# Kernel tuning notes

Measured on AMD Instinct MI355X. Metric: run time of the kernel, lower is better.

## Reference

```python
import jax, jax.numpy as jnp
import numpy as np

VOCAB, EMB_DIM, HIDDEN, NUM_CLASSES = 50000, 300, 1000, 5
B, MAX_LEN = 4096, 128


def setup_inputs() -> dict:
    key = jax.random.key(0)
    k1, k2, k3, k4, k5, k6, k7 = jax.random.split(key, 7)
    x = jax.random.randint(k1, (B, MAX_LEN), 0, VOCAB, dtype=jnp.int64)
    lengths = jnp.maximum(jax.random.randint(k2, (B,), 0, MAX_LEN, dtype=jnp.int64), 1)
    emb_table = jax.random.normal(k3, (VOCAB, EMB_DIM), dtype=jnp.float32) * 0.1
    W1 = jax.random.normal(k4, (2 * EMB_DIM, HIDDEN), dtype=jnp.float32) * (1.0 / np.sqrt(2 * EMB_DIM))
    b1 = jax.random.normal(k5, (HIDDEN,), dtype=jnp.float32) * 0.01
    W2 = jax.random.normal(k6, (HIDDEN, NUM_CLASSES), dtype=jnp.float32) * (1.0 / np.sqrt(HIDDEN))
    b2 = jax.random.normal(k7, (NUM_CLASSES,), dtype=jnp.float32) * 0.01
    return {"x": x, "lengths": lengths, "emb_table": emb_table,
            "W1": W1, "b1": b1, "W2": W2, "b2": b2}


def reference(x, lengths, emb_table, W1, b1, W2, b2):
    emb = emb_table[x]                                  # [B, L, D] gather
    mask = (jnp.arange(emb.shape[1])[None, :] < lengths[:, None])  # [B, L]
    m = mask[:, :, None].astype(emb.dtype)
    avg_pool = jnp.sum(emb * m, axis=1) / lengths[:, None].astype(emb.dtype)  # [B, D]
    neg_inf = jnp.finfo(emb.dtype).min
    max_pool = jnp.max(jnp.where(mask[:, :, None], emb, neg_inf), axis=1)     # [B, D]
    rep = jnp.concatenate([avg_pool, max_pool], axis=1)  # [B, 2D]
    hidden = jax.nn.relu(rep @ W1 + b1)                  # [B, 1000]
    logits = hidden @ W2 + b2                            # [B, C]
    return logits
```

## Files before the change

### kernel.cpp

```cpp
#include <hip/hip_runtime.h>
#include <float.h>
#include <stdint.h>

#define EMB_DIM  300
#define MAX_LEN  128
#define HIDDEN   1000
#define NCLS     5
#define VOCAB_SZ 50000
#define KPAD     640
#define NPAD     1024

typedef float    f32x4  __attribute__((ext_vector_type(4)));
typedef __bf16   bf16x8 __attribute__((ext_vector_type(8)));
typedef unsigned short ushort8v __attribute__((ext_vector_type(8)));

__device__ __forceinline__ unsigned short f2bf(float f) {
    union { float f; uint32_t u; } v; v.f = f;
    uint32_t u = v.u;
    return (unsigned short)((u + 0x7FFFu + ((u >> 16) & 1u)) >> 16);
}
__device__ __forceinline__ float bf2f(unsigned short h) {
    union { uint32_t u; float f; } v; v.u = ((uint32_t)h) << 16;
    return v.f;
}

__global__ __launch_bounds__(256) void transpose_w1(
    const float* __restrict__ W1, unsigned short* __restrict__ Bt)
{
    __shared__ float t[32][33];
    const int tx = threadIdx.x & 31, ty = threadIdx.x >> 5;
    const int n0 = blockIdx.x * 32, k0 = blockIdx.y * 32;
    #pragma unroll
    for (int i = 0; i < 4; ++i) {
        int k = k0 + ty + i * 8, n = n0 + tx;
        t[ty + i * 8][tx] = (k < 600 && n < HIDDEN) ? W1[(size_t)k * HIDDEN + n] : 0.f;
    }
    __syncthreads();
    #pragma unroll
    for (int i = 0; i < 4; ++i) {
        int n = n0 + ty + i * 8, k = k0 + tx;
        Bt[(size_t)n * KPAD + k] = f2bf(t[tx][ty + i * 8]);
    }
}

__global__ __launch_bounds__(128) void pool_kernel(
    const int* __restrict__ x, const int* __restrict__ lengths,
    const float* __restrict__ emb, unsigned short* __restrict__ rep)
{
    const int b = blockIdx.x;
    const int t = threadIdx.x;

    __shared__ int sidx[MAX_LEN];
    sidx[t] = x[b * MAX_LEN + t];
    __syncthreads();

    unsigned short* rb = rep + (size_t)b * KPAD;

    if (t >= 75) {
        if (t < 85) {
            ushort4 z = {0, 0, 0, 0};
            *(ushort4*)(rb + 600 + (t - 75) * 4) = z;
        }
        return;
    }

    int L = lengths[b];
    L = max(1, min(L, MAX_LEN));

    const int d = t * 4;
    float4 s  = {0.f, 0.f, 0.f, 0.f};
    float4 mx = {-FLT_MAX, -FLT_MAX, -FLT_MAX, -FLT_MAX};

    for (int i = 0; i < L; ++i) {
        int idx = sidx[i];
        idx = max(0, min(idx, VOCAB_SZ - 1));
        const float4 v = *(const float4*)(emb + (size_t)idx * EMB_DIM + d);
        s.x += v.x; s.y += v.y; s.z += v.z; s.w += v.w;
        mx.x = fmaxf(mx.x, v.x); mx.y = fmaxf(mx.y, v.y);
        mx.z = fmaxf(mx.z, v.z); mx.w = fmaxf(mx.w, v.w);
    }

    const float inv = 1.0f / (float)L;
    ushort4 av, mv;
    av.x = f2bf(s.x * inv); av.y = f2bf(s.y * inv);
    av.z = f2bf(s.z * inv); av.w = f2bf(s.w * inv);
    mv.x = f2bf(mx.x); mv.y = f2bf(mx.y); mv.z = f2bf(mx.z); mv.w = f2bf(mx.w);
    *(ushort4*)(rb + d)       = av;
    *(ushort4*)(rb + 300 + d) = mv;
}

#define BM 64
#define BN 64
#define BK 32

__global__ __launch_bounds__(256, 4) void gemm1_mfma(
    const unsigned short* __restrict__ A,
    const unsigned short* __restrict__ Bt,
    const float* __restrict__ bias,
    unsigned short* __restrict__ H,
    int M)
{
    __shared__ unsigned short As[2][BM * BK];
    __shared__ unsigned short Bs[2][BN * BK];

    const int tid  = threadIdx.x;
    const int wv   = tid >> 6;
    const int lane = tid & 63;
    const int bm   = blockIdx.y * BM;
    const int bn   = blockIdx.x * BN;
    const int wr   = (wv & 1) * 32;
    const int wc   = (wv >> 1) * 32;

    f32x4 acc[2][2] = {};

    auto stage = [&](int buf, int k0) {
        {
            int ci  = wv * 64 + lane;
            int row = ci >> 2, c = ci & 3;
            const unsigned short* g = A + (size_t)(bm + row) * KPAD + k0 + c * 8;
            unsigned short* l = &As[buf][wv * 512];
            __builtin_amdgcn_global_load_lds(g, l, 16, 0, 0);
        }
        {
            int ci  = wv * 64 + lane;
            int row = ci >> 2, c = ci & 3;
            const unsigned short* g = Bt + (size_t)(bn + row) * KPAD + k0 + c * 8;
            unsigned short* l = &Bs[buf][wv * 512];
            __builtin_amdgcn_global_load_lds(g, l, 16, 0, 0);
        }
    };

    stage(0, 0);
    int cur = 0;
    const int q = lane >> 4, r16 = lane & 15;

    #pragma unroll 1
    for (int it = 0; it < KPAD / BK; ++it) {
        __syncthreads();
        if (it + 1 < KPAD / BK) stage(cur ^ 1, (it + 1) * BK);

        bf16x8 af[2], bfr[2];
        #pragma unroll
        for (int mi = 0; mi < 2; ++mi)
            af[mi] = *(const bf16x8*)&As[cur][(wr + mi * 16 + r16) * BK + q * 8];
        #pragma unroll
        for (int nj = 0; nj < 2; ++nj)
            bfr[nj] = *(const bf16x8*)&Bs[cur][(wc + nj * 16 + r16) * BK + q * 8];
        #pragma unroll
        for (int mi = 0; mi < 2; ++mi)
            #pragma unroll
            for (int nj = 0; nj < 2; ++nj)
                acc[mi][nj] = __builtin_amdgcn_mfma_f32_16x16x32_bf16(
                    af[mi], bfr[nj], acc[mi][nj], 0, 0, 0);
        cur ^= 1;
    }

    #pragma unroll
    for (int nj = 0; nj < 2; ++nj) {
        int n = bn + wc + nj * 16 + r16;
        if (n >= HIDDEN) continue;
        float bv = bias[n];
        #pragma unroll
        for (int mi = 0; mi < 2; ++mi) {
            #pragma unroll
            for (int r = 0; r < 4; ++r) {
                int m = bm + wr + mi * 16 + q * 4 + r;
                float v = acc[mi][nj][r] + bv;
                H[(size_t)m * HIDDEN + n] = f2bf(fmaxf(v, 0.f));
            }
        }
    }
}

__global__ __launch_bounds__(256) void gemm2_kernel(
    const unsigned short* __restrict__ Hb,
    const float* __restrict__ W2,
    const float* __restrict__ b2,
    float* __restrict__ out)
{
    const int wv   = threadIdx.x >> 6;
    const int lane = threadIdx.x & 63;
    const int b    = blockIdx.x * 4 + wv;
    const unsigned short* hr = Hb + (size_t)b * HIDDEN;

    float acc[NCLS] = {0.f, 0.f, 0.f, 0.f, 0.f};
    #pragma unroll
    for (int c = 0; c < 2; ++c) {
        int k0 = c * 512 + lane * 8;
        if (k0 + 8 <= HIDDEN) {
            ushort8v hv = *(const ushort8v*)(hr + k0);
            #pragma unroll
            for (int j = 0; j < 8; ++j) {
                float h = bf2f(hv[j]);
                const float* w = W2 + (size_t)(k0 + j) * NCLS;
                #pragma unroll
                for (int cc = 0; cc < NCLS; ++cc) acc[cc] += h * w[cc];
            }
        }
    }
    #pragma unroll
    for (int off = 32; off > 0; off >>= 1)
        #pragma unroll
        for (int cc = 0; cc < NCLS; ++cc)
            acc[cc] += __shfl_down(acc[cc], off, 64);

    if (lane == 0) {
        #pragma unroll
        for (int cc = 0; cc < NCLS; ++cc)
            out[(size_t)b * NCLS + cc] = acc[cc] + b2[cc];
    }
}

extern "C" void kernel_launch(void* const* d_in, const int* in_sizes, int n_in,
                              void* d_out, int out_size, void* d_ws, size_t ws_size,
                              hipStream_t stream)
{
    const int*   x       = (const int*)d_in[0];
    const int*   lengths = (const int*)d_in[1];
    const float* emb     = (const float*)d_in[2];
    const float* W1      = (const float*)d_in[3];
    const float* b1      = (const float*)d_in[4];
    const float* W2      = (const float*)d_in[5];
    const float* b2      = (const float*)d_in[6];
    float*       out     = (float*)d_out;

    const int B = in_sizes[1];

    unsigned short* rep    = (unsigned short*)d_ws;
    unsigned short* w1t    = rep + (size_t)B * KPAD;
    unsigned short* hidden = w1t + (size_t)NPAD * KPAD;

    transpose_w1<<<dim3(32, 20), 256, 0, stream>>>(W1, w1t);
    pool_kernel<<<B, 128, 0, stream>>>(x, lengths, emb, rep);

    dim3 g1(NPAD / BN, B / BM);
    gemm1_mfma<<<g1, 256, 0, stream>>>(rep, w1t, b1, hidden, B);

    gemm2_kernel<<<B / 4, 256, 0, stream>>>(hidden, W2, b2, out);
}
```

Before: 167.1 us.

## Gather pooling from a bf16 copy of the embedding table and bf16 W2

```diff
diff --git a/kernel.cpp b/kernel.cpp
--- a/kernel.cpp
+++ b/kernel.cpp
@@ -9,6 +9,7 @@
 #define VOCAB_SZ 50000
 #define KPAD     640
 #define NPAD     1024
+#define EMBPAD   320
 
 typedef float    f32x4  __attribute__((ext_vector_type(4)));
 typedef __bf16   bf16x8 __attribute__((ext_vector_type(8)));
@@ -24,6 +25,22 @@
     return v.f;
 }
 
+__global__ __launch_bounds__(256) void convert_emb(
+    const float* __restrict__ emb, unsigned short* __restrict__ embb)
+{
+    const int i = blockIdx.x * 256 + threadIdx.x;
+    const int total = VOCAB_SZ * (EMBPAD / 4);
+    if (i >= total) return;
+    const int v  = i / (EMBPAD / 4);
+    const int ch = i - v * (EMBPAD / 4);
+    ushort4 o = {0, 0, 0, 0};
+    if (ch < 75) {
+        const float4 f = *(const float4*)(emb + (size_t)v * EMB_DIM + ch * 4);
+        o.x = f2bf(f.x); o.y = f2bf(f.y); o.z = f2bf(f.z); o.w = f2bf(f.w);
+    }
+    *(ushort4*)(embb + (size_t)v * EMBPAD + ch * 4) = o;
+}
+
 __global__ __launch_bounds__(256) void transpose_w1(
     const float* __restrict__ W1, unsigned short* __restrict__ Bt)
 {
@@ -43,9 +60,19 @@
     }
 }
 
-__global__ __launch_bounds__(128) void pool_kernel(
+__global__ __launch_bounds__(256) void transpose_w2(
+    const float* __restrict__ W2, unsigned short* __restrict__ W2t)
+{
+    const int i = blockIdx.x * 256 + threadIdx.x;
+    if (i >= NCLS * 1024) return;
+    const int c = i >> 10, k = i & 1023;
+    const float v = (k < HIDDEN) ? W2[(size_t)k * NCLS + c] : 0.f;
+    W2t[(size_t)c * 1024 + k] = f2bf(v);
+}
+
+__global__ __launch_bounds__(128) void pool_bf16(
     const int* __restrict__ x, const int* __restrict__ lengths,
-    const float* __restrict__ emb, unsigned short* __restrict__ rep)
+    const unsigned short* __restrict__ embb, unsigned short* __restrict__ rep)
 {
     const int b = blockIdx.x;
     const int t = threadIdx.x;
@@ -71,13 +98,25 @@
     float4 s  = {0.f, 0.f, 0.f, 0.f};
     float4 mx = {-FLT_MAX, -FLT_MAX, -FLT_MAX, -FLT_MAX};
 
-    for (int i = 0; i < L; ++i) {
-        int idx = sidx[i];
-        idx = max(0, min(idx, VOCAB_SZ - 1));
-        const float4 v = *(const float4*)(emb + (size_t)idx * EMB_DIM + d);
-        s.x += v.x; s.y += v.y; s.z += v.z; s.w += v.w;
-        mx.x = fmaxf(mx.x, v.x); mx.y = fmaxf(mx.y, v.y);
-        mx.z = fmaxf(mx.z, v.z); mx.w = fmaxf(mx.w, v.w);
+    int i = 0;
+    for (; i + 2 <= L; i += 2) {
+        int i0 = max(0, min(sidx[i],     VOCAB_SZ - 1));
+        int i1 = max(0, min(sidx[i + 1], VOCAB_SZ - 1));
+        const ushort4 a = *(const ushort4*)(embb + (size_t)i0 * EMBPAD + d);
+        const ushort4 c = *(const ushort4*)(embb + (size_t)i1 * EMBPAD + d);
+        float a0 = bf2f(a.x), a1 = bf2f(a.y), a2 = bf2f(a.z), a3 = bf2f(a.w);
+        float c0 = bf2f(c.x), c1 = bf2f(c.y), c2 = bf2f(c.z), c3 = bf2f(c.w);
+        s.x += a0 + c0; s.y += a1 + c1; s.z += a2 + c2; s.w += a3 + c3;
+        mx.x = fmaxf(mx.x, fmaxf(a0, c0)); mx.y = fmaxf(mx.y, fmaxf(a1, c1));
+        mx.z = fmaxf(mx.z, fmaxf(a2, c2)); mx.w = fmaxf(mx.w, fmaxf(a3, c3));
+    }
+    if (i < L) {
+        int i0 = max(0, min(sidx[i], VOCAB_SZ - 1));
+        const ushort4 a = *(const ushort4*)(embb + (size_t)i0 * EMBPAD + d);
+        float a0 = bf2f(a.x), a1 = bf2f(a.y), a2 = bf2f(a.z), a3 = bf2f(a.w);
+        s.x += a0; s.y += a1; s.z += a2; s.w += a3;
+        mx.x = fmaxf(mx.x, a0); mx.y = fmaxf(mx.y, a1);
+        mx.z = fmaxf(mx.z, a2); mx.w = fmaxf(mx.w, a3);
     }
 
     const float inv = 1.0f / (float)L;
@@ -89,6 +128,51 @@
     *(ushort4*)(rb + 300 + d) = mv;
 }
 
+__global__ __launch_bounds__(128) void pool_f32(
+    const int* __restrict__ x, const int* __restrict__ lengths,
+    const float* __restrict__ emb, unsigned short* __restrict__ rep)
+{
+    const int b = blockIdx.x;
+    const int t = threadIdx.x;
+
+    __shared__ int sidx[MAX_LEN];
+    sidx[t] = x[b * MAX_LEN + t];
+    __syncthreads();
+
+    unsigned short* rb = rep + (size_t)b * KPAD;
+
+    if (t >= 75) {
+        if (t < 85) {
+            ushort4 z = {0, 0, 0, 0};
+            *(ushort4*)(rb + 600 + (t - 75) * 4) = z;
+        }
+        return;
+    }
+
+    int L = lengths[b];
+    L = max(1, min(L, MAX_LEN));
+
+    const int d = t * 4;
+    float4 s  = {0.f, 0.f, 0.f, 0.f};
+    float4 mx = {-FLT_MAX, -FLT_MAX, -FLT_MAX, -FLT_MAX};
+
+    for (int i = 0; i < L; ++i) {
+        int idx = max(0, min(sidx[i], VOCAB_SZ - 1));
+        const float4 v = *(const float4*)(emb + (size_t)idx * EMB_DIM + d);
+        s.x += v.x; s.y += v.y; s.z += v.z; s.w += v.w;
+        mx.x = fmaxf(mx.x, v.x); mx.y = fmaxf(mx.y, v.y);
+        mx.z = fmaxf(mx.z, v.z); mx.w = fmaxf(mx.w, v.w);
+    }
+
+    const float inv = 1.0f / (float)L;
+    ushort4 av, mv;
+    av.x = f2bf(s.x * inv); av.y = f2bf(s.y * inv);
+    av.z = f2bf(s.z * inv); av.w = f2bf(s.w * inv);
+    mv.x = f2bf(mx.x); mv.y = f2bf(mx.y); mv.z = f2bf(mx.z); mv.w = f2bf(mx.w);
+    *(ushort4*)(rb + d)       = av;
+    *(ushort4*)(rb + 300 + d) = mv;
+}
+
 #define BM 64
 #define BN 64
 #define BK 32
@@ -174,7 +258,7 @@
 
 __global__ __launch_bounds__(256) void gemm2_kernel(
     const unsigned short* __restrict__ Hb,
-    const float* __restrict__ W2,
+    const unsigned short* __restrict__ W2t,
     const float* __restrict__ b2,
     float* __restrict__ out)
 {
@@ -189,12 +273,16 @@
         int k0 = c * 512 + lane * 8;
         if (k0 + 8 <= HIDDEN) {
             ushort8v hv = *(const ushort8v*)(hr + k0);
+            ushort8v wv8[NCLS];
+            #pragma unroll
+            for (int cc = 0; cc < NCLS; ++cc)
+                wv8[cc] = *(const ushort8v*)(W2t + cc * 1024 + k0);
             #pragma unroll
             for (int j = 0; j < 8; ++j) {
                 float h = bf2f(hv[j]);
-                const float* w = W2 + (size_t)(k0 + j) * NCLS;
                 #pragma unroll
-                for (int cc = 0; cc < NCLS; ++cc) acc[cc] += h * w[cc];
+                for (int cc = 0; cc < NCLS; ++cc)
+                    acc[cc] += h * bf2f(wv8[cc][j]);
             }
         }
     }
@@ -228,13 +316,26 @@
 
     unsigned short* rep    = (unsigned short*)d_ws;
     unsigned short* w1t    = rep + (size_t)B * KPAD;
-    unsigned short* hidden = w1t + (size_t)NPAD * KPAD;
+    unsigned short* w2t    = w1t + (size_t)NPAD * KPAD;
+    unsigned short* hidden = w2t + (size_t)NCLS * 1024;
+    unsigned short* embb   = hidden + (size_t)B * HIDDEN;
+
+    const size_t need = ((size_t)B * KPAD + (size_t)NPAD * KPAD + NCLS * 1024
+                         + (size_t)B * HIDDEN + (size_t)VOCAB_SZ * EMBPAD) * 2;
 
     transpose_w1<<<dim3(32, 20), 256, 0, stream>>>(W1, w1t);
-    pool_kernel<<<B, 128, 0, stream>>>(x, lengths, emb, rep);
+    transpose_w2<<<(NCLS * 1024 + 255) / 256, 256, 0, stream>>>(W2, w2t);
+
+    if (ws_size >= need) {
+        const int total = VOCAB_SZ * (EMBPAD / 4);
+        convert_emb<<<(total + 255) / 256, 256, 0, stream>>>(emb, embb);
+        pool_bf16<<<B, 128, 0, stream>>>(x, lengths, embb, rep);
+    } else {
+        pool_f32<<<B, 128, 0, stream>>>(x, lengths, emb, rep);
+    }
 
     dim3 g1(NPAD / BN, B / BM);
     gemm1_mfma<<<g1, 256, 0, stream>>>(rep, w1t, b1, hidden, B);
 
-    gemm2_kernel<<<B / 4, 256, 0, stream>>>(hidden, W2, b2, out);
-}
+    gemm2_kernel<<<B / 4, 256, 0, stream>>>(hidden, w2t, b2, out);
+}
```

Measured after the change: 161.3 us. 1.04x faster.
